# Kernel optimization log

Measured on AMD Instinct MI355X. Metric: run time of the kernel, lower is better.

## Reference

```python
import jax, jax.numpy as jnp
import numpy as np

H, DH, C, K = 8, 128, 200, 15  # heads, head_dim, context_size, conv kernel
SCALE = DH ** -0.5
EPS = 1e-5


def layernorm(x, g, b):
    mu = jnp.mean(x, axis=-1, keepdims=True)
    var = jnp.mean(jnp.square(x - mu), axis=-1, keepdims=True)
    return (x - mu) * jax.lax.rsqrt(var + EPS) * g + b


def feedforward(x, ln_g, ln_b, up_w, up_b, down_w, down_b):
    h = layernorm(x, ln_g, ln_b)
    h = jax.nn.silu(h @ up_w + up_b)
    return h @ down_w + down_b


def attention(x, dist, ln_g, ln_b, wq, wkv, wo, wo_b, rel_emb):
    h = layernorm(x, ln_g, ln_b)
    b, f, d = h.shape
    nb = f // C  # num_features chosen divisible by context_size (no remainder path)
    q = (h @ wq).reshape(b, nb, C, H, DH).transpose(0, 1, 3, 2, 4)   # [b,nb,H,C,dh]
    kv = h @ wkv
    k, v = jnp.split(kv, 2, axis=-1)
    k = k.reshape(b, nb, C, H, DH).transpose(0, 1, 3, 2, 4)
    v = v.reshape(b, nb, C, H, DH).transpose(0, 1, 3, 2, 4)
    rel = rel_emb[dist]                                              # [C,C,dh]
    pos_attn = jnp.einsum('bnhid,ijd->bnhij', q, rel) * SCALE
    scores = jnp.einsum('bnhid,bnhjd->bnhij', q, k) * SCALE + pos_attn
    probs = jax.nn.softmax(scores, axis=-1)
    out = jnp.einsum('bnhij,bnhjd->bnhid', probs, v)
    out = out.transpose(0, 1, 3, 2, 4).reshape(b, f, H * DH)
    return out @ wo + wo_b


def conv_module(x, ln_g, ln_b, up_w, up_b, dw_w, bn_g, bn_b, bn_mean, bn_var, down_w, down_b):
    h = layernorm(x, ln_g, ln_b)
    h = h @ up_w + up_b                         # pointwise conv == linear; [b,L,2*inner]
    a, gate = jnp.split(h, 2, axis=-1)
    h = a * jax.nn.sigmoid(gate)                # GLU over channel dim
    h = h.transpose(0, 2, 1)                    # [b,inner,L]
    pad = K // 2
    h = jax.lax.conv_general_dilated(
        h, dw_w[:, None, :], window_strides=(1,), padding=[(pad, pad)],
        dimension_numbers=('NCH', 'OIH', 'NCH'), feature_group_count=h.shape[1])
    # BatchNorm1d in eval mode (running stats)
    h = (h - bn_mean[None, :, None]) * jax.lax.rsqrt(bn_var[None, :, None] + EPS)
    h = h * bn_g[None, :, None] + bn_b[None, :, None]
    h = jax.nn.silu(h)
    h = h.transpose(0, 2, 1) @ down_w + down_b  # [b,L,hidden]
    return h


def block_forward(x, attention_dists,
                  ff1_ln_g, ff1_ln_b, ff1_up_w, ff1_up_b, ff1_down_w, ff1_down_b,
                  attn_ln_g, attn_ln_b, wq, wkv, wo, wo_b, rel_emb,
                  conv_ln_g, conv_ln_b, conv_up_w, conv_up_b, dw_w,
                  bn_g, bn_b, bn_mean, bn_var, conv_down_w, conv_down_b,
                  ff2_ln_g, ff2_ln_b, ff2_up_w, ff2_up_b, ff2_down_w, ff2_down_b,
                  post_ln_g, post_ln_b):
    x = 0.5 * feedforward(x, ff1_ln_g, ff1_ln_b, ff1_up_w, ff1_up_b, ff1_down_w, ff1_down_b) + x
    x = attention(x, attention_dists, attn_ln_g, attn_ln_b, wq, wkv, wo, wo_b, rel_emb) + x
    x = conv_module(x, conv_ln_g, conv_ln_b, conv_up_w, conv_up_b, dw_w,
                    bn_g, bn_b, bn_mean, bn_var, conv_down_w, conv_down_b) + x
    x = 0.5 * feedforward(x, ff2_ln_g, ff2_ln_b, ff2_up_w, ff2_up_b, ff2_down_w, ff2_down_b) + x
    return layernorm(x, post_ln_g, post_ln_b)


def setup_inputs() -> dict:
    key = jax.random.key(0)
    ks = iter(jax.random.split(key, 40))
    d, dff, inner = 1024, 4096, 2048
    r = lambda shape, s=0.02: (jax.random.normal(next(ks), shape, jnp.float32) * s)
    inp = {
        'x': jax.random.normal(next(ks), (8, 2000, d), jnp.float32),
        'attention_dists': jax.random.randint(next(ks), (C, C), 0, 1025, jnp.int32),
        'ff1_ln_g': jnp.ones((d,)), 'ff1_ln_b': jnp.zeros((d,)),
        'ff1_up_w': r((d, dff)), 'ff1_up_b': jnp.zeros((dff,)),
        'ff1_down_w': r((dff, d)), 'ff1_down_b': jnp.zeros((d,)),
        'attn_ln_g': jnp.ones((d,)), 'attn_ln_b': jnp.zeros((d,)),
        'wq': r((d, H * DH)), 'wkv': r((d, 2 * H * DH)),
        'wo': r((H * DH, d)), 'wo_b': jnp.zeros((d,)),
        'rel_emb': r((2 * 512 + 1, DH)),
        'conv_ln_g': jnp.ones((d,)), 'conv_ln_b': jnp.zeros((d,)),
        'conv_up_w': r((d, 2 * inner)), 'conv_up_b': jnp.zeros((2 * inner,)),
        'dw_w': r((inner, K)),
        'bn_g': jnp.ones((inner,)), 'bn_b': jnp.zeros((inner,)),
        'bn_mean': r((inner,)), 'bn_var': jax.random.uniform(next(ks), (inner,), jnp.float32) + 0.5,
        'conv_down_w': r((inner, d)), 'conv_down_b': jnp.zeros((d,)),
        'ff2_ln_g': jnp.ones((d,)), 'ff2_ln_b': jnp.zeros((d,)),
        'ff2_up_w': r((d, dff)), 'ff2_up_b': jnp.zeros((dff,)),
        'ff2_down_w': r((dff, d)), 'ff2_down_b': jnp.zeros((d,)),
        'post_ln_g': jnp.ones((d,)), 'post_ln_b': jnp.zeros((d,)),
    }
    return inp


def reference(x, attention_dists,
              ff1_ln_g, ff1_ln_b, ff1_up_w, ff1_up_b, ff1_down_w, ff1_down_b,
              attn_ln_g, attn_ln_b, wq, wkv, wo, wo_b, rel_emb,
              conv_ln_g, conv_ln_b, conv_up_w, conv_up_b, dw_w,
              bn_g, bn_b, bn_mean, bn_var, conv_down_w, conv_down_b,
              ff2_ln_g, ff2_ln_b, ff2_up_w, ff2_up_b, ff2_down_w, ff2_down_b,
              post_ln_g, post_ln_b):
    return block_forward(x, attention_dists,
                         ff1_ln_g, ff1_ln_b, ff1_up_w, ff1_up_b, ff1_down_w, ff1_down_b,
                         attn_ln_g, attn_ln_b, wq, wkv, wo, wo_b, rel_emb,
                         conv_ln_g, conv_ln_b, conv_up_w, conv_up_b, dw_w,
                         bn_g, bn_b, bn_mean, bn_var, conv_down_w, conv_down_b,
                         ff2_ln_g, ff2_ln_b, ff2_up_w, ff2_up_b, ff2_down_w, ff2_down_b,
                         post_ln_g, post_ln_b)
```

## Files before the change

kernel.cpp:

```cpp
#include <hip/hip_runtime.h>

typedef unsigned short u16;
typedef unsigned int u32;
using short8 = __attribute__((ext_vector_type(8))) short;
using floatx4 = __attribute__((ext_vector_type(4))) float;

#define DMODEL 1024
#define DFF 4096
#define INNER 2048
#define DH 128
#define CTX 200
#define R_TOT 16000
#define ABN 40
#define AROWS (ABN * CTX)
#define AM (ABN * 8)
#define SCALE_Q 0.08838834764831845f

__device__ __forceinline__ u16 f2bf(float f) {
    union { float f; u32 u; } v; v.f = f;
    u32 r = v.u + 0x7FFFu + ((v.u >> 16) & 1u);
    return (u16)(r >> 16);
}
__device__ __forceinline__ float bf2f(u16 u) {
    union { u32 u; float f; } v; v.u = ((u32)u) << 16; return v.f;
}
__device__ __forceinline__ float sigmoidf_(float x) { return 1.f / (1.f + __expf(-x)); }

__device__ __forceinline__ void load_lds16(const void* g, void* l) {
    __builtin_amdgcn_global_load_lds((const __attribute__((address_space(1))) u32*)g,
                                     (__attribute__((address_space(3))) u32*)l, 16, 0, 0);
}

__device__ __forceinline__ void xcd_stripe_remap(int& bx, int& by) {
    const int gx = gridDim.x;
    const int gxs = gx >> 3;
    const int id = blockIdx.y * gx + blockIdx.x;
    const int xcd = id & 7;
    const int local = id >> 3;
    bx = xcd * gxs + (local % gxs);
    by = local / gxs;
}

template <int MODE>
__device__ __forceinline__ void epi_store(int r, int c, float v, int M, int ldc,
                                          const float* bias, float alpha, void* out,
                                          const float* resid) {
    if (r >= M) return;
    size_t idx = (size_t)r * ldc + c;
    float bb = bias ? bias[c] : 0.f;
    if (MODE == 0) {
        ((u16*)out)[idx] = f2bf(alpha * v + bb);
    } else if (MODE == 1) {
        float t = v + bb;
        ((u16*)out)[idx] = f2bf(t * sigmoidf_(t));
    } else {
        ((float*)out)[idx] = alpha * (v + bb) + resid[idx];
    }
}

template <int MODE>
__global__ __launch_bounds__(256, 3) void k_g(const u16* __restrict__ A, int lda,
                                              const u16* __restrict__ Bt, int ldb,
                                              const float* __restrict__ bias, float alpha,
                                              void* out, int ldc, const float* resid, int M,
                                              int N, int K) {
    __shared__ __align__(128) char lds[32768];
    int bx, by;
    xcd_stripe_remap(bx, by);
    const int row0 = bx * 128, col0 = by * 128;
    if (row0 >= M) return;
    const int lane = threadIdx.x & 63;
    const int wave = threadIdx.x >> 6;
    const int wrow = (wave >> 1) * 64;
    const int wcol = (wave & 1) * 64;
    const int lr = lane & 15;
    const int kg = lane >> 4;
    const int nt = K >> 6;

    const char* sA[4];
    const char* sB[4];
#pragma unroll
    for (int r = 0; r < 4; ++r) {
        int o = r * 4096 + wave * 1024 + lane * 16;
        int row = o >> 7;
        int srcb = (o & 127) ^ ((row & 7) << 4);
        int ga = row0 + row;
        ga = (ga < M) ? ga : M - 1;
        sA[r] = (const char*)A + (size_t)ga * ((size_t)lda * 2) + srcb;
        int gb = col0 + row;
        gb = (gb < N) ? gb : N - 1;
        sB[r] = (const char*)Bt + (size_t)gb * ((size_t)ldb * 2) + srcb;
    }
    floatx4 acc[4][4];
#pragma unroll
    for (int i = 0; i < 4; ++i)
#pragma unroll
        for (int j = 0; j < 4; ++j) acc[i][j] = (floatx4){0.f, 0.f, 0.f, 0.f};

    for (int t = 0; t < nt; ++t) {
        const int kb = t << 7;
#pragma unroll
        for (int r = 0; r < 4; ++r) {
            load_lds16(sA[r] + kb, lds + r * 4096 + wave * 1024);
            load_lds16(sB[r] + kb, lds + 16384 + r * 4096 + wave * 1024);
        }
        asm volatile("s_waitcnt vmcnt(0)" ::: "memory");
        __builtin_amdgcn_s_barrier();
#pragma unroll
        for (int ks = 0; ks < 2; ++ks) {
            short8 av[4], bv[4];
#pragma unroll
            for (int mi = 0; mi < 4; ++mi) {
                int row = wrow + mi * 16 + lr;
                int cb = (ks * 64 + kg * 16) ^ ((row & 7) << 4);
                av[mi] = *(const short8*)(lds + row * 128 + cb);
            }
#pragma unroll
            for (int ni = 0; ni < 4; ++ni) {
                int row = wcol + ni * 16 + lr;
                int cb = (ks * 64 + kg * 16) ^ ((row & 7) << 4);
                bv[ni] = *(const short8*)(lds + 16384 + row * 128 + cb);
            }
#pragma unroll
            for (int mi = 0; mi < 4; ++mi)
#pragma unroll
                for (int ni = 0; ni < 4; ++ni)
                    acc[mi][ni] = __builtin_amdgcn_mfma_f32_16x16x32_bf16(av[mi], bv[ni],
                                                                          acc[mi][ni], 0, 0, 0);
        }
        asm volatile("s_waitcnt lgkmcnt(0)" ::: "memory");
        __builtin_amdgcn_s_barrier();
    }
#pragma unroll
    for (int mi = 0; mi < 4; ++mi)
#pragma unroll
        for (int ni = 0; ni < 4; ++ni)
#pragma unroll
            for (int rr = 0; rr < 4; ++rr)
                epi_store<MODE>(row0 + wrow + mi * 16 + kg * 4 + rr, col0 + wcol + ni * 16 + lr,
                                acc[mi][ni][rr], M, ldc, bias, alpha, out, resid);
}

template <typename RowMap>
__device__ __forceinline__ void stage_tile_g(const char* __restrict__ src, RowMap rowoff,
                                             int nrows, int row0, int k0b, char* tile) {
    const int lane = threadIdx.x & 63;
    const int wave = threadIdx.x >> 6;
#pragma unroll
    for (int r = 0; r < 4; ++r) {
        int o = r * 4096 + wave * 1024 + lane * 16;
        int row = o >> 7;
        int srcb = (o & 127) ^ ((row & 7) << 4);
        int grow = row0 + row;
        grow = (grow < nrows) ? grow : (nrows - 1);
        const char* g = src + rowoff(grow) + k0b + srcb;
        load_lds16(g, tile + r * 4096 + wave * 1024);
    }
}

template <typename RMA, typename RMB, typename Epi>
__device__ __forceinline__ void gemm_core_g(const char* __restrict__ A, RMA rma, int a_rows,
                                            const char* __restrict__ B, RMB rmb, int b_rows,
                                            int K, int row0, int col0, char* lds, Epi epi) {
    const int lane = threadIdx.x & 63;
    const int wave = threadIdx.x >> 6;
    const int wrow = (wave >> 1) * 64;
    const int wcol = (wave & 1) * 64;
    const int lr = lane & 15;
    const int kg = lane >> 4;
    const int nt = K >> 6;

    floatx4 acc[4][4];
#pragma unroll
    for (int i = 0; i < 4; ++i)
#pragma unroll
        for (int j = 0; j < 4; ++j) acc[i][j] = (floatx4){0.f, 0.f, 0.f, 0.f};

    stage_tile_g(A, rma, a_rows, row0, 0, lds);
    stage_tile_g(B, rmb, b_rows, col0, 0, lds + 16384);
    asm volatile("s_waitcnt vmcnt(0)" ::: "memory");
    __builtin_amdgcn_s_barrier();

    for (int t = 0; t < nt; ++t) {
        char* cur = lds + (t & 1) * 32768;
        char* nxt = lds + ((t + 1) & 1) * 32768;
        if (t + 1 < nt) {
            stage_tile_g(A, rma, a_rows, row0, (t + 1) << 7, nxt);
            stage_tile_g(B, rmb, b_rows, col0, (t + 1) << 7, nxt + 16384);
        }
#pragma unroll
        for (int ks = 0; ks < 2; ++ks) {
            short8 av[4], bv[4];
#pragma unroll
            for (int mi = 0; mi < 4; ++mi) {
                int row = wrow + mi * 16 + lr;
                int cb = (ks * 64 + kg * 16) ^ ((row & 7) << 4);
                av[mi] = *(const short8*)(cur + row * 128 + cb);
            }
#pragma unroll
            for (int ni = 0; ni < 4; ++ni) {
                int row = wcol + ni * 16 + lr;
                int cb = (ks * 64 + kg * 16) ^ ((row & 7) << 4);
                bv[ni] = *(const short8*)(cur + 16384 + row * 128 + cb);
            }
            __builtin_amdgcn_s_setprio(1);
#pragma unroll
            for (int mi = 0; mi < 4; ++mi)
#pragma unroll
                for (int ni = 0; ni < 4; ++ni)
                    acc[mi][ni] = __builtin_amdgcn_mfma_f32_16x16x32_bf16(av[mi], bv[ni],
                                                                          acc[mi][ni], 0, 0, 0);
            __builtin_amdgcn_s_setprio(0);
        }
        if (t + 1 < nt)
            asm volatile("s_waitcnt vmcnt(0) lgkmcnt(0)" ::: "memory");
        else
            asm volatile("s_waitcnt lgkmcnt(0)" ::: "memory");
        __builtin_amdgcn_sched_barrier(0);
        __builtin_amdgcn_s_barrier();
    }
#pragma unroll
    for (int mi = 0; mi < 4; ++mi)
#pragma unroll
        for (int ni = 0; ni < 4; ++ni)
#pragma unroll
            for (int rr = 0; rr < 4; ++rr)
                epi(row0 + wrow + mi * 16 + kg * 4 + rr, col0 + wcol + ni * 16 + lr,
                    acc[mi][ni][rr]);
}

__global__ __launch_bounds__(256, 2) void k_qk(const u16* __restrict__ q,
                                               const u16* __restrict__ kvc,
                                               u16* __restrict__ sc, int bn0) {
    __shared__ __align__(128) char lds[65536];
    const int z = blockIdx.z, bnl = z >> 3, h = z & 7;
    const char* A = (const char*)(q + ((size_t)(bn0 + bnl) * CTX) * DMODEL + h * DH);
    const char* B = (const char*)(kvc + ((size_t)bnl * CTX) * (2 * DMODEL) + h * DH);
    u16* out = sc + (size_t)z * CTX * 256;
    gemm_core_g(A, [](int r) { return (size_t)r * (DMODEL * 2); }, CTX, B,
                [](int r) { return (size_t)r * (4 * DMODEL); }, CTX, DH, blockIdx.x * 128,
                blockIdx.y * 128, lds, [&](int r, int c, float v) {
                    if (r < CTX) out[(size_t)r * 256 + c] = f2bf(v);
                });
}

__global__ __launch_bounds__(256, 2) void k_pos(const u16* __restrict__ q,
                                                const u16* __restrict__ rel,
                                                u16* __restrict__ sc, int m0) {
    __shared__ __align__(128) char lds[65536];
    const int i = blockIdx.z;
    const char* B = (const char*)(rel + (size_t)i * CTX * DH);
    u16* out = sc + i * 256;
    gemm_core_g((const char*)q,
                [=](int r) {
                    int m = m0 + r;
                    return (size_t)(((m >> 3) * CTX + i) * DMODEL + (m & 7) * DH) * 2;
                },
                AM, B, [](int r) { return (size_t)r * (DH * 2); }, CTX, DH, blockIdx.x * 128,
                blockIdx.y * 128, lds, [&](int r, int c, float v) {
                    if (r < AM) {
                        size_t idx = (size_t)r * (CTX * 256) + c;
                        out[idx] = f2bf(bf2f(out[idx]) + v);
                    }
                });
}

__global__ __launch_bounds__(256, 2) void k_pv(const u16* __restrict__ P,
                                               const u16* __restrict__ vT,
                                               u16* __restrict__ attn, int bn0) {
    __shared__ __align__(128) char lds[65536];
    const int z = blockIdx.z;
    u16* out = attn + ((size_t)(bn0 + (z >> 3)) * CTX) * DMODEL + (z & 7) * DH;
    const char* A = (const char*)(P + (size_t)z * CTX * 256);
    const char* B = (const char*)(vT + (size_t)z * DH * 256);
    gemm_core_g(A, [](int r) { return (size_t)r * 512; }, CTX, B,
                [](int r) { return (size_t)r * 512; }, DH, 256, blockIdx.x * 128, 0, lds,
                [&](int r, int c, float v) {
                    if (r < CTX) out[(size_t)r * DMODEL + c] = f2bf(v);
                });
}

template <bool OUTF32>
__global__ __launch_bounds__(256) void k_ln(const float* __restrict__ x,
                                            const float* __restrict__ g,
                                            const float* __restrict__ b, void* __restrict__ out) {
    const int row = blockIdx.x, t = threadIdx.x, lane = t & 63, wv = t >> 6;
    const float4 v = ((const float4*)(x + (size_t)row * DMODEL))[t];
    float s = v.x + v.y + v.z + v.w;
    float q = v.x * v.x + v.y * v.y + v.z * v.z + v.w * v.w;
#pragma unroll
    for (int off = 32; off > 0; off >>= 1) { s += __shfl_down(s, off); q += __shfl_down(q, off); }
    __shared__ float rs_[4], rq_[4];
    if (lane == 0) { rs_[wv] = s; rq_[wv] = q; }
    __syncthreads();
    s = rs_[0] + rs_[1] + rs_[2] + rs_[3];
    q = rq_[0] + rq_[1] + rq_[2] + rq_[3];
    const float mu = s * (1.f / DMODEL);
    const float rstd = rsqrtf(q * (1.f / DMODEL) - mu * mu + 1e-5f);
    const float4 gv = ((const float4*)g)[t];
    const float4 bv = ((const float4*)b)[t];
    float o0 = (v.x - mu) * rstd * gv.x + bv.x;
    float o1 = (v.y - mu) * rstd * gv.y + bv.y;
    float o2 = (v.z - mu) * rstd * gv.z + bv.z;
    float o3 = (v.w - mu) * rstd * gv.w + bv.w;
    if (OUTF32) {
        ((float4*)out)[(size_t)row * 256 + t] = make_float4(o0, o1, o2, o3);
    } else {
        ushort4 r4;
        r4.x = f2bf(o0); r4.y = f2bf(o1); r4.z = f2bf(o2); r4.w = f2bf(o3);
        ((ushort4*)out)[(size_t)row * 256 + t] = r4;
    }
}

__global__ __launch_bounds__(256) void k_softmax(u16* __restrict__ sc) {
    const size_t row = blockIdx.x;
    const int t = threadIdx.x, lane = t & 63, wv = t >> 6;
    float v = (t < CTX) ? bf2f(sc[row * 256 + t]) : -3.0e38f;
    float m = v;
#pragma unroll
    for (int off = 32; off > 0; off >>= 1) m = fmaxf(m, __shfl_down(m, off));
    __shared__ float rm[4], rsum[4];
    if (lane == 0) rm[wv] = m;
    __syncthreads();
    m = fmaxf(fmaxf(rm[0], rm[1]), fmaxf(rm[2], rm[3]));
    float e = (t < CTX) ? __expf(v - m) : 0.f;
    float s = e;
#pragma unroll
    for (int off = 32; off > 0; off >>= 1) s += __shfl_down(s, off);
    if (lane == 0) rsum[wv] = s;
    __syncthreads();
    s = rsum[0] + rsum[1] + rsum[2] + rsum[3];
    sc[row * 256 + t] = f2bf(e / s);
}

__global__ __launch_bounds__(256) void k_glu(u16* __restrict__ mid) {
    const size_t r = blockIdx.x;
    const int c = threadIdx.x * 8;
    const short8 a8 = *(const short8*)(mid + r * 4096 + c);
    const short8 g8 = *(const short8*)(mid + r * 4096 + 2048 + c);
    short8 o8;
#pragma unroll
    for (int e = 0; e < 8; ++e) {
        float av = bf2f((u16)a8[e]), gg = bf2f((u16)g8[e]);
        o8[e] = (short)f2bf(av * sigmoidf_(gg));
    }
    *(short8*)(mid + r * 4096 + c) = o8;
}

__global__ __launch_bounds__(256) void k_dwconv(const u16* __restrict__ in,
                                                const float* __restrict__ w,
                                                const float* __restrict__ bng,
                                                const float* __restrict__ bnb,
                                                const float* __restrict__ bnm,
                                                const float* __restrict__ bnv,
                                                u16* __restrict__ out) {
    const int b = blockIdx.z, lt = blockIdx.x, cg = blockIdx.y;
    const int c = cg * 256 + threadIdx.x;
    const int l0 = lt * 16;
    __shared__ u16 s[30][256];
#pragma unroll
    for (int rr = 0; rr < 30; ++rr) {
        int l = l0 + rr - 7;
        u16 v = 0;
        if (l >= 0 && l < 2000) v = in[((size_t)b * 2000 + l) * 4096 + c];
        s[rr][threadIdx.x] = v;
    }
    __syncthreads();
    float wv[15];
#pragma unroll
    for (int k = 0; k < 15; ++k) wv[k] = w[c * 15 + k];
    const float sc = rsqrtf(bnv[c] + 1e-5f) * bng[c];
    const float mean = bnm[c], bb = bnb[c];
#pragma unroll
    for (int l = 0; l < 16; ++l) {
        float acc = 0.f;
#pragma unroll
        for (int k = 0; k < 15; ++k) acc += bf2f(s[l + k][threadIdx.x]) * wv[k];
        float h = (acc - mean) * sc + bb;
        h = h * sigmoidf_(h);
        out[((size_t)b * 2000 + l0 + l) * 4096 + c] = f2bf(h);
    }
}

__global__ __launch_bounds__(256) void k_wt(const float* __restrict__ w, u16* __restrict__ wt,
                                            int K, int N) {
    __shared__ float tile[32][33];
    const int k0 = blockIdx.x * 32, n0 = blockIdx.y * 32;
    const int tx = threadIdx.x & 31, ty = threadIdx.x >> 5;
#pragma unroll
    for (int i = 0; i < 32; i += 8) tile[ty + i][tx] = w[(size_t)(k0 + ty + i) * N + n0 + tx];
    __syncthreads();
#pragma unroll
    for (int i = 0; i < 32; i += 8)
        wt[(size_t)(n0 + ty + i) * K + k0 + tx] = f2bf(tile[tx][ty + i]);
}

__global__ void k_rel(const float* __restrict__ emb, const int* __restrict__ dist,
                      u16* __restrict__ rel) {
    const int bid = blockIdx.x;
    const int d = dist[bid];
    rel[(size_t)bid * DH + threadIdx.x] = f2bf(emb[(size_t)d * DH + threadIdx.x]);
}

__global__ __launch_bounds__(256) void k_vt(const u16* __restrict__ kvc, u16* __restrict__ vT) {
    __shared__ u16 t_[64 * 130];
    const int z = blockIdx.x, jt = blockIdx.y;
    const int bnl = z >> 3, h = z & 7;
    const int j0 = jt * 64;
    for (int idx = threadIdx.x; idx < 8192; idx += 256) {
        int j = idx >> 7, dh = idx & 127;
        int jj = j0 + j;
        u16 val = 0;
        if (jj < CTX) val = kvc[((size_t)(bnl * CTX + jj)) * (2 * DMODEL) + DMODEL + h * DH + dh];
        t_[j * 130 + dh] = val;
    }
    __syncthreads();
    for (int idx = threadIdx.x; idx < 8192; idx += 256) {
        int dh = idx >> 6, j = idx & 63;
        vT[((size_t)z * DH + dh) * 256 + j0 + j] = t_[j * 130 + dh];
    }
}

__global__ void k_fill(float* o, int n, float v) {
    int i = blockIdx.x * 256 + threadIdx.x;
    if (i < n) o[i] = v;
}

extern "C" void kernel_launch(void* const* d_in, const int* in_sizes, int n_in, void* d_out,
                              int out_size, void* d_ws, size_t ws_size, hipStream_t stream) {
    const float* x_in = (const float*)d_in[0];
    const int* dists = (const int*)d_in[1];
    const float* ff1_ln_g = (const float*)d_in[2];
    const float* ff1_ln_b = (const float*)d_in[3];
    const float* ff1_up_w = (const float*)d_in[4];
    const float* ff1_up_b = (const float*)d_in[5];
    const float* ff1_down_w = (const float*)d_in[6];
    const float* ff1_down_b = (const float*)d_in[7];
    const float* attn_ln_g = (const float*)d_in[8];
    const float* attn_ln_b = (const float*)d_in[9];
    const float* wq = (const float*)d_in[10];
    const float* wkv = (const float*)d_in[11];
    const float* wo = (const float*)d_in[12];
    const float* wo_b = (const float*)d_in[13];
    const float* rel_emb = (const float*)d_in[14];
    const float* conv_ln_g = (const float*)d_in[15];
    const float* conv_ln_b = (const float*)d_in[16];
    const float* conv_up_w = (const float*)d_in[17];
    const float* conv_up_b = (const float*)d_in[18];
    const float* dw_w = (const float*)d_in[19];
    const float* bn_g = (const float*)d_in[20];
    const float* bn_b = (const float*)d_in[21];
    const float* bn_mean = (const float*)d_in[22];
    const float* bn_var = (const float*)d_in[23];
    const float* conv_down_w = (const float*)d_in[24];
    const float* conv_down_b = (const float*)d_in[25];
    const float* ff2_ln_g = (const float*)d_in[26];
    const float* ff2_ln_b = (const float*)d_in[27];
    const float* ff2_up_w = (const float*)d_in[28];
    const float* ff2_up_b = (const float*)d_in[29];
    const float* ff2_down_w = (const float*)d_in[30];
    const float* ff2_down_b = (const float*)d_in[31];
    const float* post_ln_g = (const float*)d_in[32];
    const float* post_ln_b = (const float*)d_in[33];

    char* W = (char*)d_ws;
    size_t off = 0;
    auto alloc = [&](size_t bytes) {
        char* p = W + off;
        off += (bytes + 255) & ~(size_t)255;
        return (u16*)p;
    };
    u16* slot = alloc((size_t)4096 * 1024 * 2);
    u16* ln_buf = alloc((size_t)R_TOT * DMODEL * 2);
    u16* arena = alloc((size_t)R_TOT * DFF * 2);
    u16* mid = arena;
    u16* rel_bf = arena;
    u16* bufA = rel_bf + (size_t)CTX * CTX * DH;
    u16* bufB = bufA + (size_t)AROWS * 2 * DMODEL;
    u16* smid = bufB + (size_t)R_TOT * DMODEL;
    u16* vT = smid + (size_t)AM * CTX * 256;
    float* xs = (float*)d_out;

    if (ws_size < off) {
        k_fill<<<(out_size + 255) / 256, 256, 0, stream>>>((float*)d_out, out_size, 31337.f);
        return;
    }

    auto WT = [&](const float* s, int K, int N) {
        k_wt<<<dim3(K / 32, N / 32), 256, 0, stream>>>(s, slot, K, N);
    };

    const dim3 gUP(128, 32);
    const dim3 gSQ(128, 8);
    const dim3 gKV(64, 16);

    auto ff_block = [&](const float* lng, const float* lnb, const float* upw, const float* upb,
                        const float* dnw, const float* dnb, const float* resid,
                        const float* xsrc) {
        k_ln<false><<<R_TOT, 256, 0, stream>>>(xsrc, lng, lnb, ln_buf);
        WT(upw, 1024, 4096);
        k_g<1><<<gUP, 256, 0, stream>>>(ln_buf, DMODEL, slot, DMODEL, upb, 1.f, mid, DFF,
                                        nullptr, R_TOT, DFF, DMODEL);
        WT(dnw, 4096, 1024);
        k_g<2><<<gSQ, 256, 0, stream>>>(mid, DFF, slot, DFF, dnb, 0.5f, xs, DMODEL, resid,
                                        R_TOT, DMODEL, DFF);
    };

    ff_block(ff1_ln_g, ff1_ln_b, ff1_up_w, ff1_up_b, ff1_down_w, ff1_down_b, x_in, x_in);

    k_ln<false><<<R_TOT, 256, 0, stream>>>(xs, attn_ln_g, attn_ln_b, ln_buf);
    k_rel<<<CTX * CTX, 128, 0, stream>>>(rel_emb, dists, rel_bf);
    WT(wq, 1024, 1024);
    k_g<0><<<gSQ, 256, 0, stream>>>(ln_buf, DMODEL, slot, DMODEL, nullptr, SCALE_Q, bufB,
                                    DMODEL, nullptr, R_TOT, DMODEL, DMODEL);
    WT(wkv, 1024, 2048);
    for (int h = 0; h < 2; ++h) {
        const int bn0 = h * ABN, m0 = bn0 * 8;
        const u16* lnc = ln_buf + (size_t)bn0 * CTX * DMODEL;
        k_g<0><<<gKV, 256, 0, stream>>>(lnc, DMODEL, slot, DMODEL, nullptr, 1.f, bufA,
                                        2 * DMODEL, nullptr, AROWS, 2 * DMODEL, DMODEL);
        k_vt<<<dim3(AM, 4), 256, 0, stream>>>(bufA, vT);
        k_qk<<<dim3(2, 2, AM), 256, 0, stream>>>(bufB, bufA, smid, bn0);
        k_pos<<<dim3(3, 2, CTX), 256, 0, stream>>>(bufB, rel_bf, smid, m0);
        k_softmax<<<AM * CTX, 256, 0, stream>>>(smid);
        k_pv<<<dim3(2, 1, AM), 256, 0, stream>>>(smid, vT, bufB, bn0);
    }
    WT(wo, 1024, 1024);
    k_g<2><<<gSQ, 256, 0, stream>>>(bufB, DMODEL, slot, DMODEL, wo_b, 1.f, xs, DMODEL, xs,
                                    R_TOT, DMODEL, DMODEL);

    k_ln<false><<<R_TOT, 256, 0, stream>>>(xs, conv_ln_g, conv_ln_b, ln_buf);
    WT(conv_up_w, 1024, 4096);
    k_g<0><<<gUP, 256, 0, stream>>>(ln_buf, DMODEL, slot, DMODEL, conv_up_b, 1.f, mid, DFF,
                                    nullptr, R_TOT, DFF, DMODEL);
    k_glu<<<R_TOT, 256, 0, stream>>>(mid);
    k_dwconv<<<dim3(125, 8, 8), 256, 0, stream>>>(mid, dw_w, bn_g, bn_b, bn_mean, bn_var,
                                                  mid + INNER);
    WT(conv_down_w, 2048, 1024);
    k_g<2><<<gSQ, 256, 0, stream>>>(mid + INNER, DFF, slot, INNER, conv_down_b, 1.f, xs,
                                    DMODEL, xs, R_TOT, DMODEL, INNER);

    ff_block(ff2_ln_g, ff2_ln_b, ff2_up_w, ff2_up_b, ff2_down_w, ff2_down_b, xs, xs);

    k_ln<true><<<R_TOT, 256, 0, stream>>>(xs, post_ln_g, post_ln_b, d_out);
}
```

Before: 1.704 ms.

## Single-buffer attention GEMM core to halve LDS and raise occupancy

Replaces the double-buffered LDS pipeline in the attention GEMM helper (qk, pos, pv) with a single-buffered load-wait-compute loop, halving shared memory to 32KB and raising launch bounds to 4 blocks per CU. The main GEMM kernel's launch bound also goes from 3 to 4. The aim is more resident waves so that latency is hidden through occupancy instead of software prefetch. These GEMMs have short K (128 or 256, so only 2–4 tiles), where prefetch gives little overlap. The cost is that no load/compute overlap remains inside a block, the setprio hints are dropped, and register pressure on the main GEMM may cause spills.

```diff
diff --git a/kernel.cpp b/kernel.cpp
--- a/kernel.cpp
+++ b/kernel.cpp
@@ -59,7 +59,7 @@
 }
 
 template <int MODE>
-__global__ __launch_bounds__(256, 3) void k_g(const u16* __restrict__ A, int lda,
+__global__ __launch_bounds__(256, 4) void k_g(const u16* __restrict__ A, int lda,
                                               const u16* __restrict__ Bt, int ldb,
                                               const float* __restrict__ bias, float alpha,
                                               void* out, int ldc, const float* resid, int M,
@@ -142,7 +142,7 @@
 }
 
 template <typename RowMap>
-__device__ __forceinline__ void stage_tile_g(const char* __restrict__ src, RowMap rowoff,
+__device__ __forceinline__ void stage_tile_s(const char* __restrict__ src, RowMap rowoff,
                                              int nrows, int row0, int k0b, char* tile) {
     const int lane = threadIdx.x & 63;
     const int wave = threadIdx.x >> 6;
@@ -153,13 +153,12 @@
         int srcb = (o & 127) ^ ((row & 7) << 4);
         int grow = row0 + row;
         grow = (grow < nrows) ? grow : (nrows - 1);
-        const char* g = src + rowoff(grow) + k0b + srcb;
-        load_lds16(g, tile + r * 4096 + wave * 1024);
+        load_lds16(src + rowoff(grow) + k0b + srcb, tile + r * 4096 + wave * 1024);
     }
 }
 
 template <typename RMA, typename RMB, typename Epi>
-__device__ __forceinline__ void gemm_core_g(const char* __restrict__ A, RMA rma, int a_rows,
+__device__ __forceinline__ void gemm_core_s(const char* __restrict__ A, RMA rma, int a_rows,
                                             const char* __restrict__ B, RMB rmb, int b_rows,
                                             int K, int row0, int col0, char* lds, Epi epi) {
     const int lane = threadIdx.x & 63;
@@ -176,18 +175,12 @@
 #pragma unroll
         for (int j = 0; j < 4; ++j) acc[i][j] = (floatx4){0.f, 0.f, 0.f, 0.f};
 
-    stage_tile_g(A, rma, a_rows, row0, 0, lds);
-    stage_tile_g(B, rmb, b_rows, col0, 0, lds + 16384);
-    asm volatile("s_waitcnt vmcnt(0)" ::: "memory");
-    __builtin_amdgcn_s_barrier();
-
     for (int t = 0; t < nt; ++t) {
-        char* cur = lds + (t & 1) * 32768;
-        char* nxt = lds + ((t + 1) & 1) * 32768;
-        if (t + 1 < nt) {
-            stage_tile_g(A, rma, a_rows, row0, (t + 1) << 7, nxt);
-            stage_tile_g(B, rmb, b_rows, col0, (t + 1) << 7, nxt + 16384);
-        }
+        const int kb = t << 7;
+        stage_tile_s(A, rma, a_rows, row0, kb, lds);
+        stage_tile_s(B, rmb, b_rows, col0, kb, lds + 16384);
+        asm volatile("s_waitcnt vmcnt(0)" ::: "memory");
+        __builtin_amdgcn_s_barrier();
 #pragma unroll
         for (int ks = 0; ks < 2; ++ks) {
             short8 av[4], bv[4];
@@ -195,28 +188,22 @@
             for (int mi = 0; mi < 4; ++mi) {
                 int row = wrow + mi * 16 + lr;
                 int cb = (ks * 64 + kg * 16) ^ ((row & 7) << 4);
-                av[mi] = *(const short8*)(cur + row * 128 + cb);
+                av[mi] = *(const short8*)(lds + row * 128 + cb);
             }
 #pragma unroll
             for (int ni = 0; ni < 4; ++ni) {
                 int row = wcol + ni * 16 + lr;
                 int cb = (ks * 64 + kg * 16) ^ ((row & 7) << 4);
-                bv[ni] = *(const short8*)(cur + 16384 + row * 128 + cb);
+                bv[ni] = *(const short8*)(lds + 16384 + row * 128 + cb);
             }
-            __builtin_amdgcn_s_setprio(1);
 #pragma unroll
             for (int mi = 0; mi < 4; ++mi)
 #pragma unroll
                 for (int ni = 0; ni < 4; ++ni)
                     acc[mi][ni] = __builtin_amdgcn_mfma_f32_16x16x32_bf16(av[mi], bv[ni],
                                                                           acc[mi][ni], 0, 0, 0);
-            __builtin_amdgcn_s_setprio(0);
         }
-        if (t + 1 < nt)
-            asm volatile("s_waitcnt vmcnt(0) lgkmcnt(0)" ::: "memory");
-        else
-            asm volatile("s_waitcnt lgkmcnt(0)" ::: "memory");
-        __builtin_amdgcn_sched_barrier(0);
+        asm volatile("s_waitcnt lgkmcnt(0)" ::: "memory");
         __builtin_amdgcn_s_barrier();
     }
 #pragma unroll
@@ -229,29 +216,29 @@
                     acc[mi][ni][rr]);
 }
 
-__global__ __launch_bounds__(256, 2) void k_qk(const u16* __restrict__ q,
+__global__ __launch_bounds__(256, 4) void k_qk(const u16* __restrict__ q,
                                                const u16* __restrict__ kvc,
                                                u16* __restrict__ sc, int bn0) {
-    __shared__ __align__(128) char lds[65536];
+    __shared__ __align__(128) char lds[32768];
     const int z = blockIdx.z, bnl = z >> 3, h = z & 7;
     const char* A = (const char*)(q + ((size_t)(bn0 + bnl) * CTX) * DMODEL + h * DH);
     const char* B = (const char*)(kvc + ((size_t)bnl * CTX) * (2 * DMODEL) + h * DH);
     u16* out = sc + (size_t)z * CTX * 256;
-    gemm_core_g(A, [](int r) { return (size_t)r * (DMODEL * 2); }, CTX, B,
+    gemm_core_s(A, [](int r) { return (size_t)r * (DMODEL * 2); }, CTX, B,
                 [](int r) { return (size_t)r * (4 * DMODEL); }, CTX, DH, blockIdx.x * 128,
                 blockIdx.y * 128, lds, [&](int r, int c, float v) {
                     if (r < CTX) out[(size_t)r * 256 + c] = f2bf(v);
                 });
 }
 
-__global__ __launch_bounds__(256, 2) void k_pos(const u16* __restrict__ q,
+__global__ __launch_bounds__(256, 4) void k_pos(const u16* __restrict__ q,
                                                 const u16* __restrict__ rel,
                                                 u16* __restrict__ sc, int m0) {
-    __shared__ __align__(128) char lds[65536];
+    __shared__ __align__(128) char lds[32768];
     const int i = blockIdx.z;
     const char* B = (const char*)(rel + (size_t)i * CTX * DH);
     u16* out = sc + i * 256;
-    gemm_core_g((const char*)q,
+    gemm_core_s((const char*)q,
                 [=](int r) {
                     int m = m0 + r;
                     return (size_t)(((m >> 3) * CTX + i) * DMODEL + (m & 7) * DH) * 2;
@@ -265,15 +252,15 @@
                 });
 }
 
-__global__ __launch_bounds__(256, 2) void k_pv(const u16* __restrict__ P,
+__global__ __launch_bounds__(256, 4) void k_pv(const u16* __restrict__ P,
                                                const u16* __restrict__ vT,
                                                u16* __restrict__ attn, int bn0) {
-    __shared__ __align__(128) char lds[65536];
+    __shared__ __align__(128) char lds[32768];
     const int z = blockIdx.z;
     u16* out = attn + ((size_t)(bn0 + (z >> 3)) * CTX) * DMODEL + (z & 7) * DH;
     const char* A = (const char*)(P + (size_t)z * CTX * 256);
     const char* B = (const char*)(vT + (size_t)z * DH * 256);
-    gemm_core_g(A, [](int r) { return (size_t)r * 512; }, CTX, B,
+    gemm_core_s(A, [](int r) { return (size_t)r * 512; }, CTX, B,
                 [](int r) { return (size_t)r * 512; }, DH, 256, blockIdx.x * 128, 0, lds,
                 [&](int r, int c, float v) {
                     if (r < CTX) out[(size_t)r * DMODEL + c] = f2bf(v);
```

Measured after the change: 1.672 ms, median of 2. No clear change (-1.9%).
